# Optimization experiments

Measured on AMD Instinct MI355X. Metric: run time of the kernel, lower is better.

Reference implementation:

```python
import jax, jax.numpy as jnp
import numpy as np

GROUPS = 8
BASE = 8

def conv3d(x, w, b):
    y = jax.lax.conv_general_dilated(x, w, window_strides=(1, 1, 1), padding='SAME',
                                     dimension_numbers=('NCDHW', 'OIDHW', 'NCDHW'))
    return y + b[None, :, None, None, None]


def setup_inputs() -> dict:
    key = jax.random.key(0)
    ks = jax.random.split(key, 8)
    b, M, F, C, h, w, D = 2, 2, 6, 32, 64, 64, 32
    features = jax.random.normal(ks[0], (b, M, F, C, h, w), jnp.float32)
    cameras = jax.random.normal(ks[1], (b, M, 3, 3), jnp.float32)
    to_worlds = jax.random.normal(ks[2], (b, M, 4, 4), jnp.float32)
    # sorted positive depth hypotheses in [1, 10]
    hypo_distances = jnp.sort(jax.random.uniform(ks[3], (b, D), jnp.float32), axis=1) * 9.0 + 1.0
    idx_to_process = jnp.ones((b, F), dtype=bool)
    w0 = jax.random.normal(ks[4], (BASE, GROUPS, 3, 3, 3), jnp.float32) * 0.1
    b0 = jnp.zeros((BASE,), jnp.float32)
    w1 = jax.random.normal(ks[5], (BASE, BASE, 3, 3, 3), jnp.float32) * 0.1
    b1 = jnp.zeros((BASE,), jnp.float32)
    wp = jax.random.normal(ks[6], (1, BASE, 3, 3, 3), jnp.float32) * 0.1
    bp = jnp.zeros((1,), jnp.float32)
    return {'features': features, 'cameras': cameras, 'to_worlds': to_worlds,
            'hypo_distances': hypo_distances, 'w0': w0, 'b0': b0, 'w1': w1, 'b1': b1,
            'wp': wp, 'bp': bp, 'idx_to_process': idx_to_process}


def _forward(features, cameras, to_worlds, hypo_distances, w0, b0, w1, b1, wp, bp, idx_to_process):
    b, M, F, C, h, w = features.shape  # F = 6 cube faces
    D = hypo_distances.shape[1]
    # torch: features.transpose(2,3).flatten(3,4) -> (b, M, C, 6*h, w)
    f = features.transpose(0, 1, 3, 2, 4, 5).reshape(b, M, C, F * h, w)
    # --- cost_volume stand-in (plane sweep): ref broadcast over D, src depth-modulated ---
    s_cam = jnp.tanh(jnp.mean(cameras, axis=(-2, -1)))    # (b, M)
    s_tw = jnp.tanh(jnp.mean(to_worlds, axis=(-2, -1)))   # (b, M)
    ref = f[:, :1]                                        # (b, 1, C, H, W)
    src = f[:, 1:]                                        # (b, M-1, C, H, W)
    ref_vol = jnp.broadcast_to(ref[:, :, :, None], (b, 1, C, D, F * h, w))
    phase = s_cam[:, 1:, None] * hypo_distances[:, None, :] + s_tw[:, 1:, None]  # (b, M-1, D)
    src_vols = src[:, :, :, None] * jnp.cos(phase)[:, :, None, :, None, None]    # (b, M-1, C, D, H, W)
    # unflatten 6 faces, move face dim next to batch
    ref_vol = ref_vol.reshape(b, 1, C, D, F, h, w)[:, 0].transpose(0, 3, 1, 2, 4, 5)        # (b,6,C,D,h,w)
    src_vols = src_vols.reshape(b, M - 1, C, D, F, h, w).transpose(0, 4, 1, 2, 3, 5, 6)     # (b,6,M-1,C,D,h,w)
    # --- sparse gather of faces to process ---
    idx_flat = idx_to_process.reshape(-1)                 # (b*6,) bool (all True here)
    to_process = jnp.nonzero(idx_flat, size=idx_flat.shape[0])[0]
    ref_s = ref_vol.reshape(b * F, C, D, h, w)[to_process][:, None]   # (k,1,C,D,h,w)
    src_s = src_vols.reshape(b * F, M - 1, C, D, h, w)[to_process]    # (k,M-1,C,D,h,w)
    k = ref_s.shape[0]
    Cg = C // GROUPS
    ref_s = ref_s.reshape(k, 1, GROUPS, Cg, D, h, w)
    src_s = src_s.reshape(k, M - 1, GROUPS, Cg, D, h, w)
    # group-wise mean correlation
    sim = jnp.mean(ref_s * src_s, axis=3)                 # (k, M-1, G, D, h, w)
    combined = sim[:, 0]                                  # M-1 == 1 -> squeeze
    # --- 3D cost regularization ---
    x = jax.nn.relu(conv3d(combined, w0, b0))
    x = jax.nn.relu(conv3d(x, w1, b1))
    cost = conv3d(x, wp, bp)                              # (k, 1, D, h, w)
    prob = jax.nn.softmax(cost, axis=2)
    hyp = jnp.broadcast_to(hypo_distances[:, None, :], (b, F, D)).reshape(b * F, D)[to_process]
    dist_s = jnp.sum(prob * hyp[:, None, :, None, None], axis=2)      # (k, 1, h, w)
    # scatter back to dense
    dense = jnp.zeros((b * F, 1, h, w), dist_s.dtype).at[to_process].set(dist_s)
    return dense.reshape(b, F, 1, h, w)


def reference(features, cameras, to_worlds, hypo_distances, w0, b0, w1, b1, wp, bp, idx_to_process):
    return _forward(features, cameras, to_worlds, hypo_distances, w0, b0, w1, b1, wp, bp, idx_to_process)
```

## Files before the change

kernel.cpp:

```cpp
#include <hip/hip_runtime.h>
#include <math.h>

#define B_ 2
#define M_ 2
#define F_ 6
#define C_ 32
#define H_ 64
#define W_ 64
#define D_ 32
#define K_ (B_*F_)
#define G_ 8
#define CG_ 4
#define O_ 8

__global__ void kern_cp(const float* __restrict__ cameras,
                        const float* __restrict__ to_worlds,
                        const float* __restrict__ hypo,
                        float* __restrict__ cp) {
    int t = threadIdx.x;
    if (t >= B_ * D_) return;
    int b = t / D_, d = t % D_;
    const float* cam = cameras + (size_t)(b*M_ + 1) * 9;
    float sc = 0.f;
    for (int i = 0; i < 9; i++) sc += cam[i];
    sc = tanhf(sc / 9.f);
    const float* tw = to_worlds + (size_t)(b*M_ + 1) * 16;
    float st = 0.f;
    for (int i = 0; i < 16; i++) st += tw[i];
    st = tanhf(st / 16.f);
    cp[t] = cosf(sc * hypo[b*D_ + d] + st);
}

__global__ __launch_bounds__(256) void kern_dot(const float* __restrict__ feat,
                                                float* __restrict__ dotp) {
    int idx = blockIdx.x * 256 + threadIdx.x;
    int x  = idx & 63;
    int y  = (idx >> 6) & 63;
    int g  = (idx >> 12) & 7;
    int kk = idx >> 15;
    int b = kk / F_, f = kk % F_;
    size_t base0 = ((((size_t)(b*M_ + 0)*F_ + f)*C_ + g*CG_)*H_ + y)*W_ + x;
    size_t base1 = ((((size_t)(b*M_ + 1)*F_ + f)*C_ + g*CG_)*H_ + y)*W_ + x;
    float s = 0.f;
    #pragma unroll
    for (int cg = 0; cg < CG_; cg++)
        s += feat[base0 + (size_t)cg*H_*W_] * feat[base1 + (size_t)cg*H_*W_];
    dotp[idx] = s * 0.25f;
}

__global__ __launch_bounds__(256) void kern_conv0(
    const float* __restrict__ dotp, const float* __restrict__ cp,
    const float* __restrict__ w0, const float* __restrict__ b0,
    float* __restrict__ x0) {
  __shared__ float dt[G_][18][18];
  __shared__ float cps[D_+2];
  int bx = blockIdx.x;
  int kk = bx >> 4;
  int tile = bx & 15;
  int ty0 = (tile >> 2) * 16, tx0 = (tile & 3) * 16;
  int tid = threadIdx.x;
  int ty = tid >> 4, tx = tid & 15;
  int b = kk / F_;

  for (int i = tid; i < G_*18*18; i += 256) {
    int g = i / 324, r = i % 324, yy = r / 18, xx = r % 18;
    int gy = ty0 + yy - 1, gx = tx0 + xx - 1;
    float v = 0.f;
    if (gy >= 0 && gy < H_ && gx >= 0 && gx < W_)
      v = dotp[((size_t)(kk*G_ + g)*H_ + gy)*W_ + gx];
    dt[g][yy][xx] = v;
  }
  if (tid < D_+2) cps[tid] = (tid == 0 || tid == D_+1) ? 0.f : cp[b*D_ + tid - 1];
  __syncthreads();

  float S[O_*3];
  #pragma unroll
  for (int i = 0; i < O_*3; i++) S[i] = 0.f;
  #pragma unroll
  for (int g = 0; g < G_; g++)
    #pragma unroll
    for (int dy = 0; dy < 3; dy++)
      #pragma unroll
      for (int dx = 0; dx < 3; dx++) {
        float v = dt[g][ty+dy][tx+dx];
        #pragma unroll
        for (int o = 0; o < O_; o++)
          #pragma unroll
          for (int dd = 0; dd < 3; dd++)
            S[o*3+dd] += w0[o*216 + g*27 + dd*9 + dy*3 + dx] * v;
      }

  size_t outbase = (size_t)kk*O_*D_*H_*W_ + (size_t)(ty0+ty)*W_ + (tx0+tx);
  for (int d = 0; d < D_; d++) {
    #pragma unroll
    for (int o = 0; o < O_; o++) {
      float v = b0[o] + S[o*3+0]*cps[d] + S[o*3+1]*cps[d+1] + S[o*3+2]*cps[d+2];
      x0[outbase + ((size_t)o*D_ + d)*H_*W_] = fmaxf(v, 0.f);
    }
  }
}

__global__ __launch_bounds__(256) void kern_conv1(
    const float* __restrict__ x0, const float* __restrict__ w1,
    const float* __restrict__ b1, float* __restrict__ x1) {
  __shared__ float xt[3*G_*324];
  int bx = blockIdx.x;
  int kk = bx >> 9;
  int rem = bx & 511;
  int d = rem >> 4;
  int tile = rem & 15;
  int ty0 = (tile >> 2) * 16, tx0 = (tile & 3) * 16;
  int tid = threadIdx.x, ty = tid >> 4, tx = tid & 15;

  for (int i = tid; i < 3*G_*324; i += 256) {
    int dd = i / (G_*324);
    int r  = i % (G_*324);
    int c  = r / 324; int r2 = r % 324;
    int yy = r2 / 18, xx = r2 % 18;
    int jd = d + dd - 1, gy = ty0 + yy - 1, gx = tx0 + xx - 1;
    float v = 0.f;
    if (jd >= 0 && jd < D_ && gy >= 0 && gy < H_ && gx >= 0 && gx < W_)
      v = x0[(((size_t)kk*G_ + c)*D_ + jd)*H_*W_ + (size_t)gy*W_ + gx];
    xt[i] = v;
  }
  __syncthreads();

  float acc[O_];
  #pragma unroll
  for (int o = 0; o < O_; o++) acc[o] = b1[o];
  #pragma unroll
  for (int c = 0; c < G_; c++)
    #pragma unroll
    for (int dd = 0; dd < 3; dd++)
      #pragma unroll
      for (int dy = 0; dy < 3; dy++)
        #pragma unroll
        for (int dx = 0; dx < 3; dx++) {
          float v = xt[dd*2592 + c*324 + (ty+dy)*18 + (tx+dx)];
          #pragma unroll
          for (int o = 0; o < O_; o++)
            acc[o] += w1[o*216 + c*27 + dd*9 + dy*3 + dx] * v;
        }

  size_t outbase = (((size_t)kk*O_)*D_ + d)*H_*W_ + (size_t)(ty0+ty)*W_ + (tx0+tx);
  #pragma unroll
  for (int o = 0; o < O_; o++)
    x1[outbase + (size_t)o*D_*H_*W_] = fmaxf(acc[o], 0.f);
}

__global__ __launch_bounds__(256) void kern_cost(
    const float* __restrict__ x1, const float* __restrict__ wp,
    const float* __restrict__ bp, float* __restrict__ cost) {
  __shared__ float xt[3*G_*324];
  int bx = blockIdx.x;
  int kk = bx >> 9;
  int rem = bx & 511;
  int d = rem >> 4;
  int tile = rem & 15;
  int ty0 = (tile >> 2) * 16, tx0 = (tile & 3) * 16;
  int tid = threadIdx.x, ty = tid >> 4, tx = tid & 15;

  for (int i = tid; i < 3*G_*324; i += 256) {
    int dd = i / (G_*324);
    int r  = i % (G_*324);
    int c  = r / 324; int r2 = r % 324;
    int yy = r2 / 18, xx = r2 % 18;
    int jd = d + dd - 1, gy = ty0 + yy - 1, gx = tx0 + xx - 1;
    float v = 0.f;
    if (jd >= 0 && jd < D_ && gy >= 0 && gy < H_ && gx >= 0 && gx < W_)
      v = x1[(((size_t)kk*G_ + c)*D_ + jd)*H_*W_ + (size_t)gy*W_ + gx];
    xt[i] = v;
  }
  __syncthreads();

  float acc = bp[0];
  #pragma unroll
  for (int c = 0; c < G_; c++)
    #pragma unroll
    for (int dd = 0; dd < 3; dd++)
      #pragma unroll
      for (int dy = 0; dy < 3; dy++)
        #pragma unroll
        for (int dx = 0; dx < 3; dx++)
          acc += wp[c*27 + dd*9 + dy*3 + dx]
               * xt[dd*2592 + c*324 + (ty+dy)*18 + (tx+dx)];

  cost[(((size_t)kk*D_ + d)*H_ + (ty0+ty))*W_ + (tx0+tx)] = acc;
}

__global__ __launch_bounds__(256) void kern_smax(
    const float* __restrict__ cost, const float* __restrict__ hypo,
    float* __restrict__ out) {
  int idx = blockIdx.x * 256 + threadIdx.x;
  int kk = idx >> 12;
  int px = idx & 4095;
  int b = kk / F_;
  float mx = -1e30f, ss = 0.f, ts = 0.f;
  #pragma unroll
  for (int d = 0; d < D_; d++) {
    float cst = cost[(((size_t)kk*D_ + d) << 12) + px];
    float hy  = hypo[b*D_ + d];
    float nm  = fmaxf(mx, cst);
    float scl = __expf(mx - nm);
    float e   = __expf(cst - nm);
    ss = ss*scl + e;
    ts = ts*scl + e*hy;
    mx = nm;
  }
  out[idx] = ts / ss;
}

extern "C" void kernel_launch(void* const* d_in, const int* in_sizes, int n_in,
                              void* d_out, int out_size, void* d_ws, size_t ws_size,
                              hipStream_t stream) {
    const float* features  = (const float*)d_in[0];
    const float* cameras   = (const float*)d_in[1];
    const float* to_worlds = (const float*)d_in[2];
    const float* hypo      = (const float*)d_in[3];
    const float* w0        = (const float*)d_in[4];
    const float* b0        = (const float*)d_in[5];
    const float* w1        = (const float*)d_in[6];
    const float* b1        = (const float*)d_in[7];
    const float* wp        = (const float*)d_in[8];
    const float* bp        = (const float*)d_in[9];

    float* ws   = (float*)d_ws;
    float* cp   = ws;
    float* dotp = cp + 64;
    float* x0   = dotp + (size_t)K_*G_*H_*W_;
    float* x1   = x0   + (size_t)K_*O_*D_*H_*W_;
    float* cost = x0;
    float* out  = (float*)d_out;

    kern_cp   <<<1, 64, 0, stream>>>(cameras, to_worlds, hypo, cp);
    kern_dot  <<<(K_*G_*H_*W_)/256, 256, 0, stream>>>(features, dotp);
    kern_conv0<<<K_*16, 256, 0, stream>>>(dotp, cp, w0, b0, x0);
    kern_conv1<<<K_*D_*16, 256, 0, stream>>>(x0, w1, b1, x1);
    kern_cost <<<K_*D_*16, 256, 0, stream>>>(x1, wp, bp, cost);
    kern_smax <<<(K_*H_*W_)/256, 256, 0, stream>>>(cost, hypo, out);
}
```

Baseline: 350.6 us.

## Register-block conv1 and cost kernels over 4 pixels with full-width row tiles

The conv1 and cost 3D convolution kernels now give each block a 16x64 full-width tile and each thread 4 adjacent x outputs. Each thread reuses 6 shared-memory loads across 3 dx taps and all 8 output channels. The depth-neighbour planes are staged into shared memory one slice at a time, with padded rows so float4 reads stay aligned, and outputs are written with float4 stores. This cuts LDS reads per FMA and the halo overhead, at the cost of a quarter as many blocks, more registers, and extra barriers per depth slice.

New measurement: 343.4 us. -2.0%, faster.

```diff
diff --git a/kernel.cpp b/kernel.cpp
--- a/kernel.cpp
+++ b/kernel.cpp
@@ -12,6 +12,10 @@
 #define G_ 8
 #define CG_ 4
 #define O_ 8
+
+#define ROWW 68
+#define PLANE (18*ROWW)
+#define CHUNK_ELEMS (8*18*66)
 
 __global__ void kern_cp(const float* __restrict__ cameras,
                         const float* __restrict__ to_worlds,
@@ -103,89 +107,141 @@
 __global__ __launch_bounds__(256) void kern_conv1(
     const float* __restrict__ x0, const float* __restrict__ w1,
     const float* __restrict__ b1, float* __restrict__ x1) {
-  __shared__ float xt[3*G_*324];
+  __shared__ float xt[8*PLANE];
   int bx = blockIdx.x;
-  int kk = bx >> 9;
-  int rem = bx & 511;
-  int d = rem >> 4;
-  int tile = rem & 15;
-  int ty0 = (tile >> 2) * 16, tx0 = (tile & 3) * 16;
-  int tid = threadIdx.x, ty = tid >> 4, tx = tid & 15;
-
-  for (int i = tid; i < 3*G_*324; i += 256) {
-    int dd = i / (G_*324);
-    int r  = i % (G_*324);
-    int c  = r / 324; int r2 = r % 324;
-    int yy = r2 / 18, xx = r2 % 18;
-    int jd = d + dd - 1, gy = ty0 + yy - 1, gx = tx0 + xx - 1;
-    float v = 0.f;
-    if (jd >= 0 && jd < D_ && gy >= 0 && gy < H_ && gx >= 0 && gx < W_)
-      v = x0[(((size_t)kk*G_ + c)*D_ + jd)*H_*W_ + (size_t)gy*W_ + gx];
-    xt[i] = v;
-  }
-  __syncthreads();
-
-  float acc[O_];
-  #pragma unroll
-  for (int o = 0; o < O_; o++) acc[o] = b1[o];
-  #pragma unroll
-  for (int c = 0; c < G_; c++)
-    #pragma unroll
-    for (int dd = 0; dd < 3; dd++)
-      #pragma unroll
-      for (int dy = 0; dy < 3; dy++)
+  int ytile = bx & 3;
+  int d  = (bx >> 2) & 31;
+  int kk = bx >> 7;
+  int tid = threadIdx.x;
+  int ty  = tid >> 4;
+  int x0l = (tid & 15) * 4;
+  int y0  = ytile * 16;
+
+  float acc[8][4];
+  #pragma unroll
+  for (int o = 0; o < 8; o++) {
+    float bv = b1[o];
+    #pragma unroll
+    for (int p = 0; p < 4; p++) acc[o][p] = bv;
+  }
+
+  for (int dd = 0; dd < 3; dd++) {
+    int jd = d + dd - 1;
+    bool valid = (jd >= 0) && (jd < D_);
+    if (valid) {
+      for (int i = tid; i < CHUNK_ELEMS; i += 256) {
+        int p  = i / 1188;
+        int r  = i - p*1188;
+        int rr = r / 66;
+        int cc = r - rr*66;
+        int gy = y0 + rr - 1;
+        int gx = cc - 1;
+        float v = 0.f;
+        if (gy >= 0 && gy < H_ && (unsigned)gx < (unsigned)W_)
+          v = x0[(((size_t)(kk*8 + p)*D_ + jd) << 12) + (gy << 6) + gx];
+        xt[p*PLANE + rr*ROWW + cc] = v;
+      }
+    }
+    __syncthreads();
+    if (valid) {
+      #pragma unroll 1
+      for (int c = 0; c < 8; c++) {
+        const float* wbase = w1 + c*27 + dd*9;
         #pragma unroll
-        for (int dx = 0; dx < 3; dx++) {
-          float v = xt[dd*2592 + c*324 + (ty+dy)*18 + (tx+dx)];
+        for (int dy = 0; dy < 3; dy++) {
+          const float* lp = xt + c*PLANE + (ty+dy)*ROWW + x0l;
+          float4 a03 = *(const float4*)lp;
+          float a4 = lp[4], a5 = lp[5];
+          float a[6] = {a03.x, a03.y, a03.z, a03.w, a4, a5};
           #pragma unroll
-          for (int o = 0; o < O_; o++)
-            acc[o] += w1[o*216 + c*27 + dd*9 + dy*3 + dx] * v;
+          for (int o = 0; o < 8; o++) {
+            #pragma unroll
+            for (int dx = 0; dx < 3; dx++) {
+              float wv = wbase[o*216 + dy*3 + dx];
+              #pragma unroll
+              for (int p = 0; p < 4; p++)
+                acc[o][p] += wv * a[p+dx];
+            }
+          }
         }
-
-  size_t outbase = (((size_t)kk*O_)*D_ + d)*H_*W_ + (size_t)(ty0+ty)*W_ + (tx0+tx);
-  #pragma unroll
-  for (int o = 0; o < O_; o++)
-    x1[outbase + (size_t)o*D_*H_*W_] = fmaxf(acc[o], 0.f);
+      }
+    }
+    __syncthreads();
+  }
+
+  size_t ob = (((size_t)(kk*8)*D_ + d) << 12) + ((size_t)(y0+ty) << 6) + x0l;
+  #pragma unroll
+  for (int o = 0; o < 8; o++) {
+    float4 v;
+    v.x = fmaxf(acc[o][0], 0.f); v.y = fmaxf(acc[o][1], 0.f);
+    v.z = fmaxf(acc[o][2], 0.f); v.w = fmaxf(acc[o][3], 0.f);
+    *(float4*)(x1 + ob + (((size_t)o*D_) << 12)) = v;
+  }
 }
 
 __global__ __launch_bounds__(256) void kern_cost(
     const float* __restrict__ x1, const float* __restrict__ wp,
     const float* __restrict__ bp, float* __restrict__ cost) {
-  __shared__ float xt[3*G_*324];
+  __shared__ float xt[8*PLANE];
   int bx = blockIdx.x;
-  int kk = bx >> 9;
-  int rem = bx & 511;
-  int d = rem >> 4;
-  int tile = rem & 15;
-  int ty0 = (tile >> 2) * 16, tx0 = (tile & 3) * 16;
-  int tid = threadIdx.x, ty = tid >> 4, tx = tid & 15;
-
-  for (int i = tid; i < 3*G_*324; i += 256) {
-    int dd = i / (G_*324);
-    int r  = i % (G_*324);
-    int c  = r / 324; int r2 = r % 324;
-    int yy = r2 / 18, xx = r2 % 18;
-    int jd = d + dd - 1, gy = ty0 + yy - 1, gx = tx0 + xx - 1;
-    float v = 0.f;
-    if (jd >= 0 && jd < D_ && gy >= 0 && gy < H_ && gx >= 0 && gx < W_)
-      v = x1[(((size_t)kk*G_ + c)*D_ + jd)*H_*W_ + (size_t)gy*W_ + gx];
-    xt[i] = v;
-  }
-  __syncthreads();
-
-  float acc = bp[0];
-  #pragma unroll
-  for (int c = 0; c < G_; c++)
-    #pragma unroll
-    for (int dd = 0; dd < 3; dd++)
-      #pragma unroll
-      for (int dy = 0; dy < 3; dy++)
+  int ytile = bx & 3;
+  int d  = (bx >> 2) & 31;
+  int kk = bx >> 7;
+  int tid = threadIdx.x;
+  int ty  = tid >> 4;
+  int x0l = (tid & 15) * 4;
+  int y0  = ytile * 16;
+
+  float acc[4];
+  {
+    float bv = bp[0];
+    #pragma unroll
+    for (int p = 0; p < 4; p++) acc[p] = bv;
+  }
+
+  for (int dd = 0; dd < 3; dd++) {
+    int jd = d + dd - 1;
+    bool valid = (jd >= 0) && (jd < D_);
+    if (valid) {
+      for (int i = tid; i < CHUNK_ELEMS; i += 256) {
+        int p  = i / 1188;
+        int r  = i - p*1188;
+        int rr = r / 66;
+        int cc = r - rr*66;
+        int gy = y0 + rr - 1;
+        int gx = cc - 1;
+        float v = 0.f;
+        if (gy >= 0 && gy < H_ && (unsigned)gx < (unsigned)W_)
+          v = x1[(((size_t)(kk*8 + p)*D_ + jd) << 12) + (gy << 6) + gx];
+        xt[p*PLANE + rr*ROWW + cc] = v;
+      }
+    }
+    __syncthreads();
+    if (valid) {
+      #pragma unroll 1
+      for (int c = 0; c < 8; c++) {
+        const float* wbase = wp + c*27 + dd*9;
         #pragma unroll
-        for (int dx = 0; dx < 3; dx++)
-          acc += wp[c*27 + dd*9 + dy*3 + dx]
-               * xt[dd*2592 + c*324 + (ty+dy)*18 + (tx+dx)];
-
-  cost[(((size_t)kk*D_ + d)*H_ + (ty0+ty))*W_ + (tx0+tx)] = acc;
+        for (int dy = 0; dy < 3; dy++) {
+          const float* lp = xt + c*PLANE + (ty+dy)*ROWW + x0l;
+          float4 a03 = *(const float4*)lp;
+          float a4 = lp[4], a5 = lp[5];
+          float a[6] = {a03.x, a03.y, a03.z, a03.w, a4, a5};
+          #pragma unroll
+          for (int dx = 0; dx < 3; dx++) {
+            float wv = wbase[dy*3 + dx];
+            #pragma unroll
+            for (int p = 0; p < 4; p++)
+              acc[p] += wv * a[p+dx];
+          }
+        }
+      }
+    }
+    __syncthreads();
+  }
+
+  float4 v; v.x = acc[0]; v.y = acc[1]; v.z = acc[2]; v.w = acc[3];
+  *(float4*)(cost + (((size_t)kk*D_ + d) << 12) + ((size_t)(y0+ty) << 6) + x0l) = v;
 }
 
 __global__ __launch_bounds__(256) void kern_smax(
@@ -235,7 +291,7 @@
     kern_cp   <<<1, 64, 0, stream>>>(cameras, to_worlds, hypo, cp);
     kern_dot  <<<(K_*G_*H_*W_)/256, 256, 0, stream>>>(features, dotp);
     kern_conv0<<<K_*16, 256, 0, stream>>>(dotp, cp, w0, b0, x0);
-    kern_conv1<<<K_*D_*16, 256, 0, stream>>>(x0, w1, b1, x1);
-    kern_cost <<<K_*D_*16, 256, 0, stream>>>(x1, wp, bp, cost);
+    kern_conv1<<<K_*D_*4, 256, 0, stream>>>(x0, w1, b1, x1);
+    kern_cost <<<K_*D_*4, 256, 0, stream>>>(x1, wp, bp, cost);
     kern_smax <<<(K_*H_*W_)/256, 256, 0, stream>>>(cost, hypo, out);
 }
```

## Switch intermediate volumes to depth-innermost layout and fuse cost conv with softmax

Applied to the files above, without the earlier changes.

Intermediate x0/x1 volumes are stored with depth as the innermost dimension, so each thread computes 8 consecutive depths and reads them with float4 loads straight from global memory instead of staging halo tiles in shared memory. The cost convolution and the softmax depth regression are fused into one kernel through a small shared buffer, which removes the cost tensor round trip and one launch. The dot kernel is vectorised to float4. Dropping shared-memory reuse relies on cache hits for the spatial neighbours, and the larger per-thread accumulator arrays raise register pressure.

Measured after the change: 376.6 us. 1.07x slower.

```diff
diff --git a/kernel.cpp b/kernel.cpp
--- a/kernel.cpp
+++ b/kernel.cpp
@@ -12,6 +12,7 @@
 #define G_ 8
 #define CG_ 4
 #define O_ 8
+
 
 __global__ void kern_cp(const float* __restrict__ cameras,
                         const float* __restrict__ to_worlds,
@@ -34,18 +35,23 @@
 __global__ __launch_bounds__(256) void kern_dot(const float* __restrict__ feat,
                                                 float* __restrict__ dotp) {
     int idx = blockIdx.x * 256 + threadIdx.x;
-    int x  = idx & 63;
-    int y  = (idx >> 6) & 63;
-    int g  = (idx >> 12) & 7;
-    int kk = idx >> 15;
+    int flat = idx << 2;
+    int x  = flat & 63;
+    int y  = (flat >> 6) & 63;
+    int g  = (flat >> 12) & 7;
+    int kk = flat >> 15;
     int b = kk / F_, f = kk % F_;
     size_t base0 = ((((size_t)(b*M_ + 0)*F_ + f)*C_ + g*CG_)*H_ + y)*W_ + x;
     size_t base1 = ((((size_t)(b*M_ + 1)*F_ + f)*C_ + g*CG_)*H_ + y)*W_ + x;
-    float s = 0.f;
-    #pragma unroll
-    for (int cg = 0; cg < CG_; cg++)
-        s += feat[base0 + (size_t)cg*H_*W_] * feat[base1 + (size_t)cg*H_*W_];
-    dotp[idx] = s * 0.25f;
+    float4 s = make_float4(0.f,0.f,0.f,0.f);
+    #pragma unroll
+    for (int cg = 0; cg < CG_; cg++) {
+      float4 r = *(const float4*)(feat + base0 + (size_t)cg*H_*W_);
+      float4 v = *(const float4*)(feat + base1 + (size_t)cg*H_*W_);
+      s.x += r.x*v.x; s.y += r.y*v.y; s.z += r.z*v.z; s.w += r.w*v.w;
+    }
+    s.x *= 0.25f; s.y *= 0.25f; s.z *= 0.25f; s.w *= 0.25f;
+    *(float4*)(dotp + flat) = s;
 }
 
 __global__ __launch_bounds__(256) void kern_conv0(
@@ -90,12 +96,64 @@
             S[o*3+dd] += w0[o*216 + g*27 + dd*9 + dy*3 + dx] * v;
       }
 
-  size_t outbase = (size_t)kk*O_*D_*H_*W_ + (size_t)(ty0+ty)*W_ + (tx0+tx);
-  for (int d = 0; d < D_; d++) {
-    #pragma unroll
-    for (int o = 0; o < O_; o++) {
-      float v = b0[o] + S[o*3+0]*cps[d] + S[o*3+1]*cps[d+1] + S[o*3+2]*cps[d+2];
-      x0[outbase + ((size_t)o*D_ + d)*H_*W_] = fmaxf(v, 0.f);
+  size_t pxoff = (((size_t)(ty0+ty))*W_ + (tx0+tx)) * D_;
+  #pragma unroll
+  for (int o = 0; o < O_; o++) {
+    float bv = b0[o];
+    float* op = x0 + (((size_t)kk*O_ + o) << 17) + pxoff;
+    #pragma unroll
+    for (int d4 = 0; d4 < 8; d4++) {
+      float4 v;
+      {
+        int d = d4*4;
+        v.x = fmaxf(bv + S[o*3]*cps[d+0] + S[o*3+1]*cps[d+1] + S[o*3+2]*cps[d+2], 0.f);
+        v.y = fmaxf(bv + S[o*3]*cps[d+1] + S[o*3+1]*cps[d+2] + S[o*3+2]*cps[d+3], 0.f);
+        v.z = fmaxf(bv + S[o*3]*cps[d+2] + S[o*3+1]*cps[d+3] + S[o*3+2]*cps[d+4], 0.f);
+        v.w = fmaxf(bv + S[o*3]*cps[d+3] + S[o*3+1]*cps[d+4] + S[o*3+2]*cps[d+5], 0.f);
+      }
+      *(float4*)(op + d4*4) = v;
+    }
+  }
+}
+
+template<int OUTC>
+__device__ __forceinline__ void conv3d_acc(const float* __restrict__ in,
+                                           const float* __restrict__ w,
+                                           int kk, int y, int x, int u,
+                                           float acc[OUTC][8]) {
+  int jd0 = u << 3;
+  #pragma unroll 1
+  for (int c = 0; c < 8; c++) {
+    #pragma unroll
+    for (int dy = 0; dy < 3; dy++) {
+      int gy = y + dy - 1;
+      if (gy < 0 || gy >= H_) continue;
+      const float* rowp = in + ((((size_t)kk*8 + c)*H_ + gy) << 6) * D_;
+      #pragma unroll
+      for (int dx = 0; dx < 3; dx++) {
+        int gx = x + dx - 1;
+        float in10[10];
+        #pragma unroll
+        for (int j = 0; j < 10; j++) in10[j] = 0.f;
+        if ((unsigned)gx < (unsigned)W_) {
+          const float* p = rowp + (gx << 5) + jd0;
+          float4 a  = *(const float4*)p;
+          float4 bq = *(const float4*)(p + 4);
+          in10[1]=a.x;  in10[2]=a.y;  in10[3]=a.z;  in10[4]=a.w;
+          in10[5]=bq.x; in10[6]=bq.y; in10[7]=bq.z; in10[8]=bq.w;
+          if (u > 0) in10[0] = p[-1];
+          if (u < 3) in10[9] = p[8];
+        }
+        #pragma unroll
+        for (int o = 0; o < OUTC; o++)
+          #pragma unroll
+          for (int dd = 0; dd < 3; dd++) {
+            float wv = w[o*216 + c*27 + dd*9 + dy*3 + dx];
+            #pragma unroll
+            for (int dl = 0; dl < 8; dl++)
+              acc[o][dl] += wv * in10[dl + dd];
+          }
+      }
     }
   }
 }
@@ -103,111 +161,79 @@
 __global__ __launch_bounds__(256) void kern_conv1(
     const float* __restrict__ x0, const float* __restrict__ w1,
     const float* __restrict__ b1, float* __restrict__ x1) {
-  __shared__ float xt[3*G_*324];
-  int bx = blockIdx.x;
-  int kk = bx >> 9;
-  int rem = bx & 511;
-  int d = rem >> 4;
-  int tile = rem & 15;
-  int ty0 = (tile >> 2) * 16, tx0 = (tile & 3) * 16;
-  int tid = threadIdx.x, ty = tid >> 4, tx = tid & 15;
-
-  for (int i = tid; i < 3*G_*324; i += 256) {
-    int dd = i / (G_*324);
-    int r  = i % (G_*324);
-    int c  = r / 324; int r2 = r % 324;
-    int yy = r2 / 18, xx = r2 % 18;
-    int jd = d + dd - 1, gy = ty0 + yy - 1, gx = tx0 + xx - 1;
-    float v = 0.f;
-    if (jd >= 0 && jd < D_ && gy >= 0 && gy < H_ && gx >= 0 && gx < W_)
-      v = x0[(((size_t)kk*G_ + c)*D_ + jd)*H_*W_ + (size_t)gy*W_ + gx];
-    xt[i] = v;
-  }
+  int bxx = blockIdx.x;
+  int kk = bxx >> 6;
+  int y  = bxx & 63;
+  int tid = threadIdx.x;
+  int u = tid >> 6;
+  int x = tid & 63;
+
+  float acc[8][8];
+  #pragma unroll
+  for (int o = 0; o < 8; o++) {
+    float bv = b1[o];
+    #pragma unroll
+    for (int dl = 0; dl < 8; dl++) acc[o][dl] = bv;
+  }
+
+  conv3d_acc<8>(x0, w1, kk, y, x, u, acc);
+
+  size_t pxoff = (((size_t)y << 6) + x) * D_ + (u << 3);
+  #pragma unroll
+  for (int o = 0; o < 8; o++) {
+    float* op = x1 + (((size_t)kk*8 + o) << 17) + pxoff;
+    float4 v0, v1;
+    v0.x = fmaxf(acc[o][0], 0.f); v0.y = fmaxf(acc[o][1], 0.f);
+    v0.z = fmaxf(acc[o][2], 0.f); v0.w = fmaxf(acc[o][3], 0.f);
+    v1.x = fmaxf(acc[o][4], 0.f); v1.y = fmaxf(acc[o][5], 0.f);
+    v1.z = fmaxf(acc[o][6], 0.f); v1.w = fmaxf(acc[o][7], 0.f);
+    *(float4*)op = v0;
+    *(float4*)(op + 4) = v1;
+  }
+}
+
+__global__ __launch_bounds__(256) void kern_costsmax(
+    const float* __restrict__ x1, const float* __restrict__ wp,
+    const float* __restrict__ bp, const float* __restrict__ hypo,
+    float* __restrict__ out) {
+  __shared__ float cst[4*8*64];
+  int bxx = blockIdx.x;
+  int kk = bxx >> 6;
+  int y  = bxx & 63;
+  int tid = threadIdx.x;
+  int u = tid >> 6;
+  int x = tid & 63;
+
+  float acc[1][8];
+  {
+    float bv = bp[0];
+    #pragma unroll
+    for (int dl = 0; dl < 8; dl++) acc[0][dl] = bv;
+  }
+
+  conv3d_acc<1>(x1, wp, kk, y, x, u, acc);
+
+  #pragma unroll
+  for (int dl = 0; dl < 8; dl++)
+    cst[(u << 9) + (dl << 6) + x] = acc[0][dl];
   __syncthreads();
 
-  float acc[O_];
-  #pragma unroll
-  for (int o = 0; o < O_; o++) acc[o] = b1[o];
-  #pragma unroll
-  for (int c = 0; c < G_; c++)
-    #pragma unroll
-    for (int dd = 0; dd < 3; dd++)
-      #pragma unroll
-      for (int dy = 0; dy < 3; dy++)
-        #pragma unroll
-        for (int dx = 0; dx < 3; dx++) {
-          float v = xt[dd*2592 + c*324 + (ty+dy)*18 + (tx+dx)];
-          #pragma unroll
-          for (int o = 0; o < O_; o++)
-            acc[o] += w1[o*216 + c*27 + dd*9 + dy*3 + dx] * v;
-        }
-
-  size_t outbase = (((size_t)kk*O_)*D_ + d)*H_*W_ + (size_t)(ty0+ty)*W_ + (tx0+tx);
-  #pragma unroll
-  for (int o = 0; o < O_; o++)
-    x1[outbase + (size_t)o*D_*H_*W_] = fmaxf(acc[o], 0.f);
-}
-
-__global__ __launch_bounds__(256) void kern_cost(
-    const float* __restrict__ x1, const float* __restrict__ wp,
-    const float* __restrict__ bp, float* __restrict__ cost) {
-  __shared__ float xt[3*G_*324];
-  int bx = blockIdx.x;
-  int kk = bx >> 9;
-  int rem = bx & 511;
-  int d = rem >> 4;
-  int tile = rem & 15;
-  int ty0 = (tile >> 2) * 16, tx0 = (tile & 3) * 16;
-  int tid = threadIdx.x, ty = tid >> 4, tx = tid & 15;
-
-  for (int i = tid; i < 3*G_*324; i += 256) {
-    int dd = i / (G_*324);
-    int r  = i % (G_*324);
-    int c  = r / 324; int r2 = r % 324;
-    int yy = r2 / 18, xx = r2 % 18;
-    int jd = d + dd - 1, gy = ty0 + yy - 1, gx = tx0 + xx - 1;
-    float v = 0.f;
-    if (jd >= 0 && jd < D_ && gy >= 0 && gy < H_ && gx >= 0 && gx < W_)
-      v = x1[(((size_t)kk*G_ + c)*D_ + jd)*H_*W_ + (size_t)gy*W_ + gx];
-    xt[i] = v;
-  }
-  __syncthreads();
-
-  float acc = bp[0];
-  #pragma unroll
-  for (int c = 0; c < G_; c++)
-    #pragma unroll
-    for (int dd = 0; dd < 3; dd++)
-      #pragma unroll
-      for (int dy = 0; dy < 3; dy++)
-        #pragma unroll
-        for (int dx = 0; dx < 3; dx++)
-          acc += wp[c*27 + dd*9 + dy*3 + dx]
-               * xt[dd*2592 + c*324 + (ty+dy)*18 + (tx+dx)];
-
-  cost[(((size_t)kk*D_ + d)*H_ + (ty0+ty))*W_ + (tx0+tx)] = acc;
-}
-
-__global__ __launch_bounds__(256) void kern_smax(
-    const float* __restrict__ cost, const float* __restrict__ hypo,
-    float* __restrict__ out) {
-  int idx = blockIdx.x * 256 + threadIdx.x;
-  int kk = idx >> 12;
-  int px = idx & 4095;
-  int b = kk / F_;
-  float mx = -1e30f, ss = 0.f, ts = 0.f;
-  #pragma unroll
-  for (int d = 0; d < D_; d++) {
-    float cst = cost[(((size_t)kk*D_ + d) << 12) + px];
-    float hy  = hypo[b*D_ + d];
-    float nm  = fmaxf(mx, cst);
-    float scl = __expf(mx - nm);
-    float e   = __expf(cst - nm);
-    ss = ss*scl + e;
-    ts = ts*scl + e*hy;
-    mx = nm;
-  }
-  out[idx] = ts / ss;
+  if (tid < 64) {
+    int b = kk / F_;
+    float mx = -1e30f, ss = 0.f, ts = 0.f;
+    #pragma unroll
+    for (int d = 0; d < D_; d++) {
+      float c  = cst[((d >> 3) << 9) + ((d & 7) << 6) + tid];
+      float hy = hypo[b*D_ + d];
+      float nm  = fmaxf(mx, c);
+      float scl = __expf(mx - nm);
+      float e   = __expf(c - nm);
+      ss = ss*scl + e;
+      ts = ts*scl + e*hy;
+      mx = nm;
+    }
+    out[((size_t)kk << 12) + (y << 6) + tid] = ts / ss;
+  }
 }
 
 extern "C" void kernel_launch(void* const* d_in, const int* in_sizes, int n_in,
@@ -229,13 +255,11 @@
     float* dotp = cp + 64;
     float* x0   = dotp + (size_t)K_*G_*H_*W_;
     float* x1   = x0   + (size_t)K_*O_*D_*H_*W_;
-    float* cost = x0;
     float* out  = (float*)d_out;
 
-    kern_cp   <<<1, 64, 0, stream>>>(cameras, to_worlds, hypo, cp);
-    kern_dot  <<<(K_*G_*H_*W_)/256, 256, 0, stream>>>(features, dotp);
-    kern_conv0<<<K_*16, 256, 0, stream>>>(dotp, cp, w0, b0, x0);
-    kern_conv1<<<K_*D_*16, 256, 0, stream>>>(x0, w1, b1, x1);
-    kern_cost <<<K_*D_*16, 256, 0, stream>>>(x1, wp, bp, cost);
-    kern_smax <<<(K_*H_*W_)/256, 256, 0, stream>>>(cost, hypo, out);
-}
+    kern_cp      <<<1, 64, 0, stream>>>(cameras, to_worlds, hypo, cp);
+    kern_dot     <<<(K_*G_*H_*W_/4)/256, 256, 0, stream>>>(features, dotp);
+    kern_conv0   <<<K_*16, 256, 0, stream>>>(dotp, cp, w0, b0, x0);
+    kern_conv1   <<<K_*H_, 256, 0, stream>>>(x0, w1, b1, x1);
+    kern_costsmax<<<K_*H_, 256, 0, stream>>>(x1, wp, bp, hypo, out);
+}
```
